# Kernel optimization log

Hardware: AMD Instinct MI355X
Metric: run time of the kernel (lower is better)

## Reference

```python
import jax, jax.numpy as jnp
import numpy as np

B, T_IN, T_OUT, R = 32, 128, 500, 5
MEM_D, ATT, DEC, MEL, SPEC = 256, 256, 256, 128, 513
SPK_N, SPK_D = 5, 32
N_STYLE, STYLE_D, STYLE_ATT = 10, 2, 2
STEPS = T_OUT // R


def _gru(x, h, Wg, bg, Wc, bc):
    # TF GRUCell: r,u gates then candidate with reset-gated state
    gates = jax.nn.sigmoid(jnp.concatenate([x, h], -1) @ Wg + bg)
    r, u = jnp.split(gates, 2, axis=-1)
    c = jnp.tanh(jnp.concatenate([x, r * h], -1) @ Wc + bc)
    return u * h + (1.0 - u) * c


def setup_inputs() -> dict:
    key = jax.random.key(0)
    ks = iter(jax.random.split(key, 48))
    def nrm(shape, s=0.05):
        return (jax.random.normal(next(ks), shape) * s).astype(jnp.float32)
    return dict(
        encoder_output=nrm((B, T_IN, MEM_D), 1.0),
        style_token=nrm((N_STYLE, STYLE_D), 1.0),
        mel_gtruth=nrm((B, T_OUT, MEL), 1.0),
        speaker=jax.random.randint(next(ks), (B,), 0, SPK_N),
        inp_mask=jax.random.randint(next(ks), (B,), T_IN // 2, T_IN + 1),
        spk_embed=nrm((SPK_N, SPK_D)),
        Wp1=nrm((MEL, 256)), bp1=jnp.zeros((256,), jnp.float32),
        Wp2=nrm((256, 128)), bp2=jnp.zeros((128,), jnp.float32),
        Wg_att=nrm((128 + SPK_D + ATT, 2 * ATT)), bg_att=jnp.ones((2 * ATT,), jnp.float32),
        Wc_att=nrm((128 + SPK_D + ATT, ATT)), bc_att=jnp.zeros((ATT,), jnp.float32),
        Wk=nrm((MEM_D, ATT)), Wq=nrm((ATT, ATT)), v_att=nrm((ATT,)),
        Ws_pre=nrm((STYLE_D, STYLE_D)), bs_pre=jnp.zeros((STYLE_D,), jnp.float32),
        Wk_s=nrm((STYLE_D, STYLE_ATT)), Wq_s=nrm((ATT, STYLE_ATT)), v_s=nrm((STYLE_ATT,)),
        Wa=nrm((ATT + SPK_D + MEM_D + STYLE_D, DEC)), ba=jnp.zeros((DEC,), jnp.float32),
        Wg1=nrm((2 * DEC, 2 * DEC)), bg1=jnp.ones((2 * DEC,), jnp.float32),
        Wc1=nrm((2 * DEC, DEC)), bc1=jnp.zeros((DEC,), jnp.float32),
        Wg2=nrm((2 * DEC, 2 * DEC)), bg2=jnp.ones((2 * DEC,), jnp.float32),
        Wc2=nrm((2 * DEC, DEC)), bc2=jnp.zeros((DEC,), jnp.float32),
        Wo=nrm((DEC, MEL * R)), bo=jnp.zeros((MEL * R,), jnp.float32),
        Wspec=nrm((MEL, SPEC)), bspec=jnp.zeros((SPEC,), jnp.float32),
    )


def reference(encoder_output, style_token, mel_gtruth, speaker, inp_mask, spk_embed,
              Wp1, bp1, Wp2, bp2, Wg_att, bg_att, Wc_att, bc_att,
              Wk, Wq, v_att, Ws_pre, bs_pre, Wk_s, Wq_s, v_s,
              Wa, ba, Wg1, bg1, Wc1, bc1, Wg2, bg2, Wc2, bc2,
              Wo, bo, Wspec, bspec):
    mask = jnp.arange(T_IN)[None, :] < inp_mask[:, None]          # [B, T_in]
    keys = encoder_output @ Wk                                     # precomputed attention keys [B,T_in,ATT]
    spk = spk_embed[speaker]                                       # [B, 32]
    mem_style = jax.nn.relu(style_token @ Ws_pre + bs_pre)         # style pre-net [10, 2]
    keys_s = mem_style @ Wk_s                                      # [10, 2]
    # teacher forcing: frame fed at step t is indic[r*t + r - 1] = last gt frame of previous group
    mel_t = jnp.transpose(mel_gtruth, (1, 0, 2))                   # [T_out, B, MEL]
    last = mel_t[R - 1::R]                                         # [STEPS, B, MEL]
    prev = jnp.concatenate([jnp.zeros((1, B, MEL), mel_gtruth.dtype), last[:-1]], 0)

    def step(carry, frame):
        h_att, h1, h2 = carry
        # decoder pre-net (dropout disabled: is_training=False)
        p = jax.nn.relu(frame @ Wp1 + bp1)
        p = jax.nn.relu(p @ Wp2 + bp2)
        h_att = _gru(jnp.concatenate([p, spk], -1), h_att, Wg_att, bg_att, Wc_att, bc_att)
        q = h_att
        # content attention (Bahdanau) over encoder memory
        e = jnp.einsum('bta,a->bt', jnp.tanh(keys + (q @ Wq)[:, None, :]), v_att)
        alpha = jax.nn.softmax(jnp.where(mask, e, -1e9), axis=-1)
        context = jnp.einsum('bt,btd->bd', alpha, encoder_output)
        # style attention over 10 style tokens
        e_s = jnp.einsum('bna,a->bn', jnp.tanh(keys_s[None, :, :] + (q @ Wq_s)[:, None, :]), v_s)
        alpha_s = jax.nn.softmax(e_s, axis=-1)
        context_s = alpha_s @ mem_style                            # [B, 2]
        aco_in = jnp.concatenate([h_att, spk, context, context_s], -1) @ Wa + ba
        # two residual-wrapped GRU layers
        h1n = _gru(aco_in, h1, Wg1, bg1, Wc1, bc1)
        y1 = h1n + aco_in
        h2n = _gru(y1, h2, Wg2, bg2, Wc2, bc2)
        y2 = h2n + y1
        return (h_att, h1n, h2n), (y2 @ Wo + bo, alpha)

    init = (jnp.zeros((B, ATT), jnp.float32),
            jnp.zeros((B, DEC), jnp.float32),
            jnp.zeros((B, DEC), jnp.float32))
    _, (outs, alphas) = jax.lax.scan(step, init, prev)
    output_mel = jnp.transpose(outs, (1, 0, 2)).reshape(B, T_OUT, MEL)
    output_spec = output_mel @ Wspec + bspec
    final_alpha = jnp.transpose(alphas, (1, 0, 2))                 # [B, STEPS, T_in]
    return output_mel, output_spec, final_alpha
```

## Files before the change

kernel.cpp:

```cpp
#include <hip/hip_runtime.h>

typedef unsigned short ushort_t;
typedef unsigned int   uint_t;
typedef unsigned long long u64;
typedef __attribute__((ext_vector_type(8))) short  bf16x8;
typedef __attribute__((ext_vector_type(4))) float  f32x4;

#define B_      32
#define TIN_    128
#define TOUT_   500
#define R_      5
#define STEPS_  100
#define MEL_    128
#define SPEC_   513
#define NWG_    32

#define ZB_SLOTS   0
#define ZB_AH      8192
#define ZB_ARH     24576
#define ZB_AHC     40960
#define ZB_AXH1    73728
#define ZB_AXRH1   106496
#define ZB_AY1H2   139264
#define ZB_AY1RH2  172032
#define ZB_QBUF    204800
#define ZB_UBUF    221184
#define ZB_U1BUF   253952
#define ZB_U2BUF   286720
#define ZB_EBUF    319488
#define ZB_QSBUF   335872
#define ZB_END     435200
#define OFF_SPK2    501760
#define OFF_ACOSPK2 505856
#define OFF_MS2     538624
#define OFF_KS2     539136
#define OFF_PREG2   539648
#define OFF_PREC2   7093248
#define OFF_Y2G     10370048
#define OFF_KEYSP   13646848
#define OFF_ENCP    15744000

__device__ __forceinline__ float bf1(ushort_t u){ return __uint_as_float(((uint_t)u) << 16); }
__device__ __forceinline__ ushort_t f2bf(float f){
    uint_t b = __float_as_uint(f);
    uint_t r = (b + 0x7fffu + ((b >> 16) & 1u)) >> 16;
    return (ushort_t)r;
}
__device__ __forceinline__ float fexp2(float x){ return __builtin_amdgcn_exp2f(x); }
__device__ __forceinline__ float frcp(float x){ return __builtin_amdgcn_rcpf(x); }
__device__ __forceinline__ float sigm_f(float x){ return frcp(1.f + fexp2(-1.44269504f * x)); }
__device__ __forceinline__ float tanh_f(float x){
    float e = fexp2(2.88539008f * x);
    return 1.f - 2.f * frcp(e + 1.f);
}
__device__ __forceinline__ u64 ld8(const void* p){
    return __hip_atomic_load((const u64*)p, __ATOMIC_RELAXED, __HIP_MEMORY_SCOPE_AGENT);
}
__device__ __forceinline__ void st8(void* p, u64 v){
    __hip_atomic_store((u64*)p, v, __ATOMIC_RELAXED, __HIP_MEMORY_SCOPE_AGENT);
}
__device__ __forceinline__ float ld4f(const void* p){
    uint_t u = __hip_atomic_load((const uint_t*)p, __ATOMIC_RELAXED, __HIP_MEMORY_SCOPE_AGENT);
    return __uint_as_float(u);
}
__device__ __forceinline__ void st4f(void* p, float v){
    __hip_atomic_store((uint_t*)p, __float_as_uint(v), __ATOMIC_RELAXED, __HIP_MEMORY_SCOPE_AGENT);
}
__device__ __forceinline__ float u64lo(u64 v){ return __uint_as_float((uint_t)v); }
__device__ __forceinline__ float u64hi(u64 v){ return __uint_as_float((uint_t)(v >> 32)); }
__device__ __forceinline__ u64 pack4(const ushort_t* q){
    return (u64)q[0] | ((u64)q[1] << 16) | ((u64)q[2] << 32) | ((u64)q[3] << 48);
}
__device__ __forceinline__ u64 pack2f(const float* f){
    return (u64)__float_as_uint(f[0]) | ((u64)__float_as_uint(f[1]) << 32);
}
#define CBAR() asm volatile("" ::: "memory")

__global__ __launch_bounds__(256) void k_small(
    const float* __restrict__ st, const float* __restrict__ Ws_pre,
    const float* __restrict__ bs_pre, const float* __restrict__ Wk_s,
    const float* __restrict__ spk_embed, const int* __restrict__ speaker,
    const float* __restrict__ Wa, const float* __restrict__ ba,
    float* __restrict__ spk_sel, float* __restrict__ aco_spk,
    float* __restrict__ ms_g, float* __restrict__ ks_g)
{
    __shared__ float spk_l[B_*32];
    __shared__ float ms_l[20];
    const int tid = threadIdx.x;
    for(int i=tid; i<B_*32; i+=256){
        int b = i >> 5, j = i & 31;
        float v = spk_embed[speaker[b]*32 + j];
        spk_l[i] = v; spk_sel[i] = v;
    }
    if(tid < 20){
        int n = tid >> 1, j = tid & 1;
        float v = st[n*2]*Ws_pre[j] + st[n*2+1]*Ws_pre[2+j] + bs_pre[j];
        v = fmaxf(v, 0.f);
        ms_l[tid] = v; ms_g[tid] = v;
    }
    __syncthreads();
    if(tid < 20){
        int n = tid >> 1, j = tid & 1;
        ks_g[tid] = ms_l[n*2]*Wk_s[j] + ms_l[n*2+1]*Wk_s[2+j];
    }
    for(int i=tid; i<B_*256; i+=256){
        int b = i >> 8, n = i & 255;
        float acc = ba[n];
        #pragma unroll
        for(int k=0;k<32;++k) acc = fmaf(spk_l[b*32+k], Wa[(256+k)*256 + n], acc);
        aco_spk[i] = acc;
    }
}

__global__ __launch_bounds__(256) void k_keys(const float* __restrict__ enc,
                                              const float* __restrict__ Wk,
                                              ushort_t* __restrict__ keysp){
    __shared__ float x16[16][256];
    const int bid = blockIdx.x;
    const int b = bid >> 3, tg = bid & 7, t0 = tg*16;
    const int tid = threadIdx.x;
    for(int i=tid; i<16*256; i+=256){
        int r = i >> 8, k = i & 255;
        x16[r][k] = enc[((size_t)b*TIN_ + t0 + r)*256 + k];
    }
    __syncthreads();
    float acc[16];
    #pragma unroll
    for(int r=0;r<16;++r) acc[r] = 0.f;
    for(int k=0;k<256;++k){
        float w = Wk[k*256 + tid];
        #pragma unroll
        for(int r=0;r<16;++r) acc[r] = fmaf(x16[r][k], w, acc[r]);
    }
    #pragma unroll
    for(int r=0;r<16;++r){
        int t = t0 + r;
        keysp[((size_t)((t>>2)*32 + b)*4 + (t&3))*256 + tid] = f2bf(acc[r]);
    }
}

__global__ __launch_bounds__(256) void k_encperm(const float* __restrict__ enc,
                                                 ushort_t* __restrict__ encp){
    int o = blockIdx.x*256 + threadIdx.x;
    int j = o & 7, t = (o>>3) & 127, b = (o>>10) & 31, wg = o >> 15;
    encp[o] = f2bf(enc[((size_t)b*TIN_ + t)*256 + wg*8 + j]);
}

__global__ __launch_bounds__(256) void k_prenet(
    const float* __restrict__ mg, const float* __restrict__ spk_sel,
    const float* __restrict__ Wp1, const float* __restrict__ bp1,
    const float* __restrict__ Wp2, const float* __restrict__ bp2,
    const float* __restrict__ Wg_att, const float* __restrict__ bg_att,
    const float* __restrict__ Wc_att, const float* __restrict__ bc_att,
    float* __restrict__ preg, float* __restrict__ prec)
{
    __shared__ float fr[16][128];
    __shared__ float p1[16][256];
    __shared__ float p2[16][128];
    __shared__ float spk_l[16][32];
    const int r0 = blockIdx.x * 16;
    const int tid = threadIdx.x;
    for(int i=tid; i<16*128; i+=256){
        int r = i >> 7, mcol = i & 127;
        int row = r0 + r, s = row >> 5, b = row & 31;
        fr[r][mcol] = (s == 0) ? 0.f : mg[((size_t)b*TOUT_ + s*R_ - 1)*MEL_ + mcol];
    }
    for(int i=tid; i<16*32; i+=256){
        int r = i >> 5, j = i & 31;
        spk_l[r][j] = spk_sel[((r0 + r) & 31)*32 + j];
    }
    __syncthreads();
    {
        float acc[16];
        #pragma unroll
        for(int r=0;r<16;++r) acc[r]=0.f;
        for(int k=0;k<128;++k){
            float w = Wp1[k*256 + tid];
            #pragma unroll
            for(int r=0;r<16;++r) acc[r] = fmaf(fr[r][k], w, acc[r]);
        }
        float bb = bp1[tid];
        #pragma unroll
        for(int r=0;r<16;++r) p1[r][tid] = fmaxf(acc[r] + bb, 0.f);
    }
    __syncthreads();
    if(tid < 128){
        float acc[16];
        #pragma unroll
        for(int r=0;r<16;++r) acc[r]=0.f;
        for(int k=0;k<256;++k){
            float w = Wp2[k*128 + tid];
            #pragma unroll
            for(int r=0;r<16;++r) acc[r] = fmaf(p1[r][k], w, acc[r]);
        }
        float bb = bp2[tid];
        #pragma unroll
        for(int r=0;r<16;++r) p2[r][tid] = fmaxf(acc[r] + bb, 0.f);
    }
    __syncthreads();
    {
        float aA[16], aB[16];
        #pragma unroll
        for(int r=0;r<16;++r){ aA[r]=0.f; aB[r]=0.f; }
        for(int k=0;k<128;++k){
            float wA = Wg_att[k*512 + tid], wB = Wg_att[k*512 + tid + 256];
            #pragma unroll
            for(int r=0;r<16;++r){ float pv = p2[r][k]; aA[r]=fmaf(pv,wA,aA[r]); aB[r]=fmaf(pv,wB,aB[r]); }
        }
        for(int k=0;k<32;++k){
            float wA = Wg_att[(128+k)*512 + tid], wB = Wg_att[(128+k)*512 + tid + 256];
            #pragma unroll
            for(int r=0;r<16;++r){ float sv = spk_l[r][k]; aA[r]=fmaf(sv,wA,aA[r]); aB[r]=fmaf(sv,wB,aB[r]); }
        }
        float bA = bg_att[tid], bB = bg_att[tid + 256];
        #pragma unroll
        for(int r=0;r<16;++r){
            preg[(size_t)(r0+r)*512 + tid]       = aA[r] + bA;
            preg[(size_t)(r0+r)*512 + tid + 256] = aB[r] + bB;
        }
    }
    {
        float acc[16];
        #pragma unroll
        for(int r=0;r<16;++r) acc[r]=0.f;
        for(int k=0;k<128;++k){
            float w = Wc_att[k*256 + tid];
            #pragma unroll
            for(int r=0;r<16;++r) acc[r] = fmaf(p2[r][k], w, acc[r]);
        }
        for(int k=0;k<32;++k){
            float w = Wc_att[(128+k)*256 + tid];
            #pragma unroll
            for(int r=0;r<16;++r) acc[r] = fmaf(spk_l[r][k], w, acc[r]);
        }
        float bb = bc_att[tid];
        #pragma unroll
        for(int r=0;r<16;++r) prec[(size_t)(r0+r)*256 + tid] = acc[r] + bb;
    }
}

__device__ __forceinline__ void gridbar(int* slots, int p, int seq, int tid){
    asm volatile("s_waitcnt vmcnt(0)" ::: "memory");
    __syncthreads();
    if(tid == 0)
        __hip_atomic_store(&slots[p*32], seq, __ATOMIC_RELAXED, __HIP_MEMORY_SCOPE_AGENT);
    if(tid < NWG_){
        while(__hip_atomic_load(&slots[tid*32], __ATOMIC_RELAXED, __HIP_MEMORY_SCOPE_AGENT) < seq)
            __builtin_amdgcn_s_sleep(1);
    }
    __syncthreads();
}

__device__ __forceinline__ void loadW(const float* W, int ldw, int rowbase, int nk, int kbase,
                                      int Ktot, int col0, int ncols, ushort_t* lds, int tid){
    for(int e = tid; e < 16*nk; e += 512){
        int col = e & 15, k = e >> 4;
        ushort_t v = 0;
        if(col < ncols) v = f2bf(W[(size_t)(rowbase + k)*ldw + col0 + col]);
        lds[(col*Ktot + kbase + k) ^ ((col & 7) << 3)] = v;
    }
}

template<int K>
__device__ __forceinline__ f32x4 do_gemm(const ushort_t* Ab, const ushort_t* Wl, float* red,
                                         int m, int kq, int lane){
    const int row = m*16 + (lane & 15);
    const int col = lane & 15;
    const int ko  = (lane >> 4) * 8;
    u64 av[K/64];
    #pragma unroll
    for(int t = 0; t < K/128; ++t){
        const int k0 = kq*(K/4) + t*32 + ko;
        av[2*t]   = ld8(Ab + row*K + k0);
        av[2*t+1] = ld8(Ab + row*K + k0 + 4);
    }
    f32x4 acc = {0.f,0.f,0.f,0.f};
    #pragma unroll
    for(int t = 0; t < K/128; ++t){
        const int k0 = kq*(K/4) + t*32 + ko;
        union { u64 q[2]; bf16x8 v; } ua;
        ua.q[0] = av[2*t]; ua.q[1] = av[2*t+1];
        bf16x8 b = *reinterpret_cast<const bf16x8*>(Wl + ((col*K + k0) ^ ((col & 7) << 3)));
        acc = __builtin_amdgcn_mfma_f32_16x16x32_bf16(ua.v, b, acc, 0, 0, 0);
    }
    if(kq > 0) *reinterpret_cast<f32x4*>(red + ((kq-1)*2 + m)*256 + lane*4) = acc;
    __syncthreads();
    if(kq == 0){
        #pragma unroll
        for(int j = 0; j < 3; ++j)
            acc += *reinterpret_cast<const f32x4*>(red + (j*2 + m)*256 + lane*4);
    }
    return acc;
}

__global__ __launch_bounds__(512) void k_scan_coop(
    char* ws,
    const float* __restrict__ Wg_att, const float* __restrict__ Wc_att,
    const float* __restrict__ Wq, const float* __restrict__ Wq_s,
    const float* __restrict__ v_att, const float* __restrict__ v_s,
    const float* __restrict__ Wa,
    const float* __restrict__ Wg1, const float* __restrict__ Wc1,
    const float* __restrict__ Wg2, const float* __restrict__ Wc2,
    const float* __restrict__ bg1, const float* __restrict__ bc1,
    const float* __restrict__ bg2, const float* __restrict__ bc2,
    const int* __restrict__ inp_mask, float* __restrict__ out_alpha)
{
    const int p = blockIdx.x, tid = threadIdx.x;
    const int lane = tid & 63, wv = tid >> 6;
    const int m = wv & 1, kq = wv >> 1;

    int* slots       = (int*)(ws + ZB_SLOTS);
    ushort_t* A_h    = (ushort_t*)(ws + ZB_AH);
    ushort_t* A_rh   = (ushort_t*)(ws + ZB_ARH);
    ushort_t* A_hc   = (ushort_t*)(ws + ZB_AHC);
    ushort_t* A_xh1  = (ushort_t*)(ws + ZB_AXH1);
    ushort_t* A_xrh1 = (ushort_t*)(ws + ZB_AXRH1);
    ushort_t* A_y1h2 = (ushort_t*)(ws + ZB_AY1H2);
    ushort_t* A_y1rh2= (ushort_t*)(ws + ZB_AY1RH2);
    ushort_t* Qbuf   = (ushort_t*)(ws + ZB_QBUF);
    float* ubuf  = (float*)(ws + ZB_UBUF);
    float* u1buf = (float*)(ws + ZB_U1BUF);
    float* u2buf = (float*)(ws + ZB_U2BUF);
    float* ebuf  = (float*)(ws + ZB_EBUF);
    float* qsbuf = (float*)(ws + ZB_QSBUF);
    const float* acospk = (const float*)(ws + OFF_ACOSPK2);
    const float* msg    = (const float*)(ws + OFF_MS2);
    const float* ksg    = (const float*)(ws + OFF_KS2);
    const float* preg   = (const float*)(ws + OFF_PREG2);
    const float* prec   = (const float*)(ws + OFF_PREC2);
    float* y2g          = (float*)(ws + OFF_Y2G);
    const ushort_t* keysp = (const ushort_t*)(ws + OFF_KEYSP);
    const ushort_t* encp  = (const ushort_t*)(ws + OFF_ENCP);

    __shared__ ushort_t wA[16*256], wB[16*256], wC[16*256];
    __shared__ ushort_t wG[16*512], wH[16*512], wI[16*512], wJ[16*512], wK[16*512];
    __shared__ __align__(16) char uni[16384];
    float* red = (float*)uni;
    ushort_t* qlds = (ushort_t*)uni;
    ushort_t* stg  = (ushort_t*)(uni + 8192);
    float*    stgf = (float*)(uni + 10240);
    __shared__ float vatt_l[256];
    __shared__ float msks[48];
    __shared__ float ctxs_l[64];
    __shared__ float acosl[256], acofl[256], y1fl[256];
    __shared__ float hfl[256], h1fl[256], h2fl[256];
    __shared__ float bg1s[16], bc1s[8], bg2s[16], bc2s[8], wasl[16];
    __shared__ float wqs_l[512];
    __shared__ int   maskl[32];

    loadW(Wg_att, 512, 160, 256, 0, 256, p*16, 16, wA, tid);
    loadW(Wc_att, 256, 160, 256, 0, 256, p*8,  8,  wB, tid);
    loadW(Wq,     256, 0,   256, 0, 256, p*8,  8,  wC, tid);
    loadW(Wa,     256, 0,   256, 0,   512, p*8, 8, wG, tid);
    loadW(Wa,     256, 288, 256, 256, 512, p*8, 8, wG, tid);
    loadW(Wg1,    512, 0,   512, 0, 512, p*16, 16, wH, tid);
    loadW(Wc1,    256, 0,   512, 0, 512, p*8,  8,  wI, tid);
    loadW(Wg2,    512, 0,   512, 0, 512, p*16, 16, wJ, tid);
    loadW(Wc2,    256, 0,   512, 0, 512, p*8,  8,  wK, tid);
    if(tid < 256){
        vatt_l[tid] = v_att[tid];
        acosl[tid]  = acospk[(tid>>3)*256 + p*8 + (tid&7)];
        hfl[tid] = 0.f; h1fl[tid] = 0.f; h2fl[tid] = 0.f;
    }
    wqs_l[tid] = Wq_s[tid];
    if(tid < 20) msks[tid] = msg[tid];
    if(tid >= 20 && tid < 40) msks[tid] = ksg[tid-20];
    if(tid == 40) msks[40] = v_s[0];
    if(tid == 41) msks[41] = v_s[1];
    if(tid < 16){ bg1s[tid] = bg1[p*16+tid]; bg2s[tid] = bg2[p*16+tid]; }
    if(tid < 8){ bc1s[tid] = bc1[p*8+tid]; bc2s[tid] = bc2[p*8+tid]; }
    if(tid < 16) wasl[tid] = Wa[(size_t)(544 + (tid & 1))*256 + p*8 + (tid >> 1)];
    if(tid < 32) maskl[tid] = inp_mask[tid];
    __syncthreads();

    int seq = 0;
    for(int s = 0; s < STEPS_; ++s){
        const int sb = s*32;
        const int col = lane & 15;
        const int bbase = m*16 + ((lane>>4)<<2);
        __syncthreads();
        u64 hpre[4];
        if(kq == 0 && p < 16){
            #pragma unroll
            for(int r=0;r<4;++r) hpre[r] = ld8(A_h + (bbase+r)*256 + ((p*16+col) & ~3));
        }
        f32x4 acc = do_gemm<256>(A_h, wA, red, m, kq, lane);
        if(kq == 0){
            const int gcol = p*16 + col;
            if(p < 16){
                #pragma unroll
                for(int r=0;r<4;++r){
                    int b = bbase + r;
                    float g = sigm_f(acc[r] + preg[(size_t)(sb + b)*512 + gcol]);
                    float hb = bf1((ushort_t)(hpre[r] >> ((col & 3)*16)));
                    stg[b*16 + col] = f2bf(g * hb);
                }
                CBAR();
                int c = lane, row2 = m*16 + (c>>2), cg = c & 3;
                st8(A_rh + row2*256 + p*16 + cg*4, pack4(stg + row2*16 + cg*4));
            } else {
                #pragma unroll
                for(int r=0;r<4;++r){
                    int b = bbase + r;
                    stgf[b*16 + col] = sigm_f(acc[r] + preg[(size_t)(sb + b)*512 + gcol]);
                }
                CBAR();
                #pragma unroll
                for(int j=0;j<2;++j){
                    int c = lane*2 + j, row2 = m*16 + (c>>3), cg = c & 7;
                    st8(ubuf + row2*256 + (p-16)*16 + cg*2, pack2f(stgf + row2*16 + cg*2));
                }
            }
        }
        gridbar(slots, p, ++seq, tid);
        float upre[4];
        if(kq == 0 && col < 8){
            #pragma unroll
            for(int r=0;r<4;++r) upre[r] = ld4f(ubuf + (bbase+r)*256 + p*8 + col);
        }
        acc = do_gemm<256>(A_rh, wB, red, m, kq, lane);
        if(kq == 0){
            if(col < 8){
                const int gcol = p*8 + col;
                #pragma unroll
                for(int r=0;r<4;++r){
                    int b = bbase + r;
                    float cc = tanh_f(acc[r] + prec[(size_t)(sb + b)*256 + gcol]);
                    float u  = upre[r];
                    float hn = u*hfl[b*8 + col] + (1.f - u)*cc;
                    hfl[b*8 + col] = hn;
                    stg[b*8 + col] = f2bf(hn);
                }
            }
            CBAR();
            if(lane < 32){
                int c = lane, row2 = m*16 + (c>>1), cg = c & 1;
                u64 v = pack4(stg + row2*8 + cg*4);
                st8(A_h  + row2*256 + p*8 + cg*4, v);
                st8(A_hc + row2*512 + p*8 + cg*4, v);
            }
        }
        gridbar(slots, p, ++seq, tid);
        acc = do_gemm<256>(A_h, wC, red, m, kq, lane);
        if(kq == 0){
            if(col < 8){
                #pragma unroll
                for(int r=0;r<4;++r) stg[(bbase+r)*8 + col] = f2bf(acc[r]);
            }
            CBAR();
            if(lane < 32){
                int c = lane, row2 = m*16 + (c>>1), cg = c & 1;
                st8(Qbuf + row2*256 + p*8 + cg*4, pack4(stg + row2*8 + cg*4));
            }
        }
        if(p == 0){
            int b = tid >> 4, i = tid & 15;
            float q0 = 0.f, q1 = 0.f;
            #pragma unroll
            for(int jc=0;jc<4;++jc){
                u64 h4 = ld8(A_h + b*256 + i*16 + jc*4);
                #pragma unroll
                for(int j=0;j<4;++j){
                    int k = i*16 + jc*4 + j;
                    float hv = bf1((ushort_t)(h4 >> (j*16)));
                    q0 = fmaf(hv, wqs_l[k*2],   q0);
                    q1 = fmaf(hv, wqs_l[k*2+1], q1);
                }
            }
            #pragma unroll
            for(int d=1; d<16; d<<=1){ q0 += __shfl_xor(q0,d,64); q1 += __shfl_xor(q1,d,64); }
            if(i == 0){
                union{ float f[2]; u64 q; } pr; pr.f[0]=q0; pr.f[1]=q1;
                st8(qsbuf + b*2, pr.q);
            }
        }
        gridbar(slots, p, ++seq, tid);
        {
            u64* ql = (u64*)qlds;
            const u64* Qb = (const u64*)Qbuf;
            #pragma unroll
            for(int j=0;j<4;++j) ql[tid + j*512] = ld8(Qb + tid + j*512);
        }
        __syncthreads();
        {
            int b = tid >> 4, tl = (tid >> 2) & 3, q = tid & 3;
            int tg = p*4 + tl;
            const ushort_t* kp = keysp + (((size_t)p*32 + b)*4 + tl)*256 + q*64;
            const ushort_t* qp = qlds + b*256 + q*64;
            float e = 0.f;
            #pragma unroll
            for(int i2=0;i2<8;++i2){
                bf16x8 kv = *(const bf16x8*)(kp + i2*8);
                bf16x8 qv = *(const bf16x8*)(qp + i2*8);
                #pragma unroll
                for(int j=0;j<8;++j){
                    int a = q*64 + i2*8 + j;
                    e = fmaf(vatt_l[a], tanh_f(bf1((ushort_t)kv[j]) + bf1((ushort_t)qv[j])), e);
                }
            }
            e += __shfl_xor(e, 1, 64); e += __shfl_xor(e, 2, 64);
            if(q == 0) st4f(ebuf + b*128 + tg, (tg < maskl[b]) ? e : -1e9f);
        }
        gridbar(slots, p, ++seq, tid);
        {
            int b = tid >> 4, i = tid & 15;
            u64 ea = ld8(ebuf + b*128 + i*8);
            u64 eb = ld8(ebuf + b*128 + i*8 + 2);
            u64 ec = ld8(ebuf + b*128 + i*8 + 4);
            u64 ed = ld8(ebuf + b*128 + i*8 + 6);
            float ev[8] = { u64lo(ea),u64hi(ea),u64lo(eb),u64hi(eb),
                            u64lo(ec),u64hi(ec),u64lo(ed),u64hi(ed) };
            float mx = ev[0];
            #pragma unroll
            for(int j=1;j<8;++j) mx = fmaxf(mx, ev[j]);
            #pragma unroll
            for(int d=1; d<16; d<<=1) mx = fmaxf(mx, __shfl_xor(mx,d,64));
            float a8[8]; float sum = 0.f;
            #pragma unroll
            for(int j=0;j<8;++j){ a8[j] = fexp2((ev[j]-mx)*1.44269504f); sum += a8[j]; }
            #pragma unroll
            for(int d=1; d<16; d<<=1) sum += __shfl_xor(sum,d,64);
            float inv = frcp(sum);
            #pragma unroll
            for(int j=0;j<8;++j) a8[j] *= inv;
            if(p == 1){
                float* oa = out_alpha + ((size_t)b*STEPS_ + s)*TIN_ + i*8;
                #pragma unroll
                for(int j=0;j<8;++j) oa[j] = a8[j];
            }
            float cj[8] = {0,0,0,0,0,0,0,0};
            const ushort_t* ep = encp + (((size_t)p*32 + b)*128 + i*8)*8;
            #pragma unroll
            for(int t2=0;t2<8;++t2){
                bf16x8 ev2 = *(const bf16x8*)(ep + t2*8);
                #pragma unroll
                for(int j=0;j<8;++j) cj[j] = fmaf(a8[t2], bf1((ushort_t)ev2[j]), cj[j]);
            }
            #pragma unroll
            for(int d=1; d<16; d<<=1){
                #pragma unroll
                for(int j=0;j<8;++j) cj[j] += __shfl_xor(cj[j],d,64);
            }
            if(i == 0){
                union{ ushort_t s4[4]; u64 q; } pk0, pk1;
                #pragma unroll
                for(int j=0;j<4;++j){ pk0.s4[j] = f2bf(cj[j]); pk1.s4[j] = f2bf(cj[4+j]); }
                st8(A_hc + b*512 + 256 + p*8,     pk0.q);
                st8(A_hc + b*512 + 256 + p*8 + 4, pk1.q);
            }
        }
        if(tid < 32){
            int b = tid;
            u64 qq = ld8(qsbuf + b*2);
            float q0 = u64lo(qq), q1 = u64hi(qq);
            float es[10]; float mx = -1e30f;
            #pragma unroll
            for(int n=0;n<10;++n){
                float t = msks[40]*tanh_f(msks[20+n*2] + q0) + msks[41]*tanh_f(msks[20+n*2+1] + q1);
                es[n] = t; mx = fmaxf(mx, t);
            }
            float sum = 0.f;
            #pragma unroll
            for(int n=0;n<10;++n){ float pe = fexp2((es[n]-mx)*1.44269504f); es[n]=pe; sum += pe; }
            float inv = frcp(sum); float c0=0.f, c1=0.f;
            #pragma unroll
            for(int n=0;n<10;++n){ float al = es[n]*inv; c0 = fmaf(al, msks[n*2], c0); c1 = fmaf(al, msks[n*2+1], c1); }
            ctxs_l[b*2] = c0; ctxs_l[b*2+1] = c1;
        }
        gridbar(slots, p, ++seq, tid);
        acc = do_gemm<512>(A_hc, wG, red, m, kq, lane);
        if(kq == 0){
            if(col < 8){
                #pragma unroll
                for(int r=0;r<4;++r){
                    int b = bbase + r;
                    float v = acc[r] + acosl[b*8 + col]
                            + ctxs_l[b*2]   * wasl[col*2]
                            + ctxs_l[b*2+1] * wasl[col*2+1];
                    acofl[b*8 + col] = v;
                    stg[b*8 + col] = f2bf(v);
                }
            }
            CBAR();
            if(lane < 32){
                int c = lane, row2 = m*16 + (c>>1), cg = c & 1;
                u64 v = pack4(stg + row2*8 + cg*4);
                st8(A_xh1  + row2*512 + p*8 + cg*4, v);
                st8(A_xrh1 + row2*512 + p*8 + cg*4, v);
            }
        }
        gridbar(slots, p, ++seq, tid);
        if(kq == 0 && p < 16){
            #pragma unroll
            for(int r=0;r<4;++r) hpre[r] = ld8(A_xh1 + (bbase+r)*512 + 256 + ((p*16+col) & ~3));
        }
        acc = do_gemm<512>(A_xh1, wH, red, m, kq, lane);
        if(kq == 0){
            if(p < 16){
                #pragma unroll
                for(int r=0;r<4;++r){
                    int b = bbase + r;
                    float g = sigm_f(acc[r] + bg1s[col]);
                    float hb = bf1((ushort_t)(hpre[r] >> ((col & 3)*16)));
                    stg[b*16 + col] = f2bf(g * hb);
                }
                CBAR();
                int c = lane, row2 = m*16 + (c>>2), cg = c & 3;
                st8(A_xrh1 + row2*512 + 256 + p*16 + cg*4, pack4(stg + row2*16 + cg*4));
            } else {
                #pragma unroll
                for(int r=0;r<4;++r)
                    stgf[(bbase+r)*16 + col] = sigm_f(acc[r] + bg1s[col]);
                CBAR();
                #pragma unroll
                for(int j=0;j<2;++j){
                    int c = lane*2 + j, row2 = m*16 + (c>>3), cg = c & 7;
                    st8(u1buf + row2*256 + (p-16)*16 + cg*2, pack2f(stgf + row2*16 + cg*2));
                }
            }
        }
        gridbar(slots, p, ++seq, tid);
        if(kq == 0 && col < 8){
            #pragma unroll
            for(int r=0;r<4;++r) upre[r] = ld4f(u1buf + (bbase+r)*256 + p*8 + col);
        }
        acc = do_gemm<512>(A_xrh1, wI, red, m, kq, lane);
        if(kq == 0){
            if(col < 8){
                #pragma unroll
                for(int r=0;r<4;++r){
                    int b = bbase + r;
                    float cc = tanh_f(acc[r] + bc1s[col]);
                    float u  = upre[r];
                    float hn = u*h1fl[b*8 + col] + (1.f - u)*cc;
                    h1fl[b*8 + col] = hn;
                    stg[b*8 + col] = f2bf(hn);
                    float y1 = hn + acofl[b*8 + col];
                    y1fl[b*8 + col] = y1;
                    stg[256 + b*8 + col] = f2bf(y1);
                }
            }
            CBAR();
            if(lane < 32){
                int c = lane, row2 = m*16 + (c>>1), cg = c & 1;
                u64 vh = pack4(stg + row2*8 + cg*4);
                u64 vy = pack4(stg + 256 + row2*8 + cg*4);
                st8(A_xh1   + row2*512 + 256 + p*8 + cg*4, vh);
                st8(A_y1h2  + row2*512 + p*8 + cg*4, vy);
                st8(A_y1rh2 + row2*512 + p*8 + cg*4, vy);
            }
        }
        gridbar(slots, p, ++seq, tid);
        if(kq == 0 && p < 16){
            #pragma unroll
            for(int r=0;r<4;++r) hpre[r] = ld8(A_y1h2 + (bbase+r)*512 + 256 + ((p*16+col) & ~3));
        }
        acc = do_gemm<512>(A_y1h2, wJ, red, m, kq, lane);
        if(kq == 0){
            if(p < 16){
                #pragma unroll
                for(int r=0;r<4;++r){
                    int b = bbase + r;
                    float g = sigm_f(acc[r] + bg2s[col]);
                    float hb = bf1((ushort_t)(hpre[r] >> ((col & 3)*16)));
                    stg[b*16 + col] = f2bf(g * hb);
                }
                CBAR();
                int c = lane, row2 = m*16 + (c>>2), cg = c & 3;
                st8(A_y1rh2 + row2*512 + 256 + p*16 + cg*4, pack4(stg + row2*16 + cg*4));
            } else {
                #pragma unroll
                for(int r=0;r<4;++r)
                    stgf[(bbase+r)*16 + col] = sigm_f(acc[r] + bg2s[col]);
                CBAR();
                #pragma unroll
                for(int j=0;j<2;++j){
                    int c = lane*2 + j, row2 = m*16 + (c>>3), cg = c & 7;
                    st8(u2buf + row2*256 + (p-16)*16 + cg*2, pack2f(stgf + row2*16 + cg*2));
                }
            }
        }
        gridbar(slots, p, ++seq, tid);
        if(kq == 0 && col < 8){
            #pragma unroll
            for(int r=0;r<4;++r) upre[r] = ld4f(u2buf + (bbase+r)*256 + p*8 + col);
        }
        acc = do_gemm<512>(A_y1rh2, wK, red, m, kq, lane);
        if(kq == 0){
            if(col < 8){
                const int gcol = p*8 + col;
                #pragma unroll
                for(int r=0;r<4;++r){
                    int b = bbase + r;
                    float cc = tanh_f(acc[r] + bc2s[col]);
                    float u  = upre[r];
                    float hn = u*h2fl[b*8 + col] + (1.f - u)*cc;
                    h2fl[b*8 + col] = hn;
                    stg[b*8 + col] = f2bf(hn);
                    y2g[((size_t)sb + b)*256 + gcol] = hn + y1fl[b*8 + col];
                }
            }
            CBAR();
            if(lane < 32){
                int c = lane, row2 = m*16 + (c>>1), cg = c & 1;
                st8(A_y1h2 + row2*512 + 256 + p*8 + cg*4, pack4(stg + row2*8 + cg*4));
            }
        }
    }
}

__global__ __launch_bounds__(256) void k_omel(const float* __restrict__ y2g,
                                              const float* __restrict__ Wo,
                                              const float* __restrict__ bo,
                                              float* __restrict__ out_mel){
    __shared__ float y8[8][256];
    const int r0 = blockIdx.x * 8;
    const int tid = threadIdx.x;
    for(int i=tid; i<8*256; i+=256){ int r=i>>8, k=i&255; y8[r][k] = y2g[(size_t)(r0+r)*256 + k]; }
    __syncthreads();
    float aA[8], aB[8], aC[8];
    #pragma unroll
    for(int r=0;r<8;++r){ aA[r]=0.f; aB[r]=0.f; aC[r]=0.f; }
    for(int k=0;k<256;++k){
        float wA = Wo[(size_t)k*640 + tid];
        float wB = Wo[(size_t)k*640 + tid + 256];
        float wC = (tid < 128) ? Wo[(size_t)k*640 + tid + 512] : 0.f;
        #pragma unroll
        for(int r=0;r<8;++r){
            float yv = y8[r][k];
            aA[r]=fmaf(yv,wA,aA[r]); aB[r]=fmaf(yv,wB,aB[r]); aC[r]=fmaf(yv,wC,aC[r]);
        }
    }
    float bA = bo[tid], bB = bo[tid+256], bC = (tid<128)? bo[tid+512] : 0.f;
    #pragma unroll
    for(int r=0;r<8;++r){
        int row = r0 + r, s = row >> 5, b = row & 31;
        int mm = tid & 127;
        out_mel[((size_t)b*TOUT_ + s*R_ + (tid>>7))*MEL_ + mm]     = aA[r] + bA;
        out_mel[((size_t)b*TOUT_ + s*R_ + 2 + (tid>>7))*MEL_ + mm] = aB[r] + bB;
        if(tid < 128)
            out_mel[((size_t)b*TOUT_ + s*R_ + 4)*MEL_ + tid]       = aC[r] + bC;
    }
}

__global__ __launch_bounds__(256) void k_spec(const float* __restrict__ out_mel,
                                              const float* __restrict__ Wspec,
                                              const float* __restrict__ bspec,
                                              float* __restrict__ out_spec){
    __shared__ float m8[8][128];
    const int r0 = blockIdx.x * 8;
    const int tid = threadIdx.x;
    for(int i=tid; i<8*128; i+=256){ int r=i>>7, k=i&127; m8[r][k] = out_mel[(size_t)(r0+r)*128 + k]; }
    __syncthreads();
    float aA[8], aB[8], aC[8];
    #pragma unroll
    for(int r=0;r<8;++r){ aA[r]=0.f; aB[r]=0.f; aC[r]=0.f; }
    for(int k=0;k<128;++k){
        float wA = Wspec[(size_t)k*SPEC_ + tid];
        float wB = Wspec[(size_t)k*SPEC_ + 256 + tid];
        float wC = (tid == 0) ? Wspec[(size_t)k*SPEC_ + 512] : 0.f;
        #pragma unroll
        for(int r=0;r<8;++r){
            float mv = m8[r][k];
            aA[r]=fmaf(mv,wA,aA[r]); aB[r]=fmaf(mv,wB,aB[r]); aC[r]=fmaf(mv,wC,aC[r]);
        }
    }
    float bA = bspec[tid], bB = bspec[256+tid];
    #pragma unroll
    for(int r=0;r<8;++r){
        size_t row = (size_t)(r0 + r);
        out_spec[row*SPEC_ + tid]       = aA[r] + bA;
        out_spec[row*SPEC_ + 256 + tid] = aB[r] + bB;
        if(tid == 0) out_spec[row*SPEC_ + 512] = aC[r] + bspec[512];
    }
}

extern "C" void kernel_launch(void* const* d_in, const int* in_sizes, int n_in,
                              void* d_out, int out_size, void* d_ws, size_t ws_size,
                              hipStream_t stream) {
    const float* enc       = (const float*)d_in[0];
    const float* st        = (const float*)d_in[1];
    const float* mg        = (const float*)d_in[2];
    const int*   speaker   = (const int*)  d_in[3];
    const int*   inp_mask  = (const int*)  d_in[4];
    const float* spk_embed = (const float*)d_in[5];
    const float* Wp1=(const float*)d_in[6],  *bp1=(const float*)d_in[7];
    const float* Wp2=(const float*)d_in[8],  *bp2=(const float*)d_in[9];
    const float* Wg_att=(const float*)d_in[10], *bg_att=(const float*)d_in[11];
    const float* Wc_att=(const float*)d_in[12], *bc_att=(const float*)d_in[13];
    const float* Wk=(const float*)d_in[14], *Wq=(const float*)d_in[15], *v_att=(const float*)d_in[16];
    const float* Ws_pre=(const float*)d_in[17], *bs_pre=(const float*)d_in[18];
    const float* Wk_s=(const float*)d_in[19], *Wq_s=(const float*)d_in[20], *v_s=(const float*)d_in[21];
    const float* Wa=(const float*)d_in[22], *ba=(const float*)d_in[23];
    const float* Wg1=(const float*)d_in[24], *bg1=(const float*)d_in[25];
    const float* Wc1=(const float*)d_in[26], *bc1=(const float*)d_in[27];
    const float* Wg2=(const float*)d_in[28], *bg2=(const float*)d_in[29];
    const float* Wc2=(const float*)d_in[30], *bc2=(const float*)d_in[31];
    const float* Wo=(const float*)d_in[32], *bo=(const float*)d_in[33];
    const float* Wspec=(const float*)d_in[34], *bspec=(const float*)d_in[35];

    float* out       = (float*)d_out;
    float* out_mel   = out;
    float* out_spec  = out + 2048000;
    float* out_alpha = out + 10256000;

    char* ws = (char*)d_ws;
    float*    spk_sel = (float*)(ws + OFF_SPK2);
    float*    aco_spk = (float*)(ws + OFF_ACOSPK2);
    float*    ms_g    = (float*)(ws + OFF_MS2);
    float*    ks_g    = (float*)(ws + OFF_KS2);
    float*    preg    = (float*)(ws + OFF_PREG2);
    float*    prec    = (float*)(ws + OFF_PREC2);
    float*    y2g     = (float*)(ws + OFF_Y2G);
    ushort_t* keysp   = (ushort_t*)(ws + OFF_KEYSP);
    ushort_t* encp    = (ushort_t*)(ws + OFF_ENCP);

    hipMemsetAsync(d_ws, 0, ZB_END, stream);

    k_small<<<dim3(1), dim3(256), 0, stream>>>(st, Ws_pre, bs_pre, Wk_s, spk_embed,
                                               speaker, Wa, ba, spk_sel, aco_spk, ms_g, ks_g);
    k_keys   <<<dim3(256),  dim3(256), 0, stream>>>(enc, Wk, keysp);
    k_encperm<<<dim3(4096), dim3(256), 0, stream>>>(enc, encp);
    k_prenet <<<dim3(200),  dim3(256), 0, stream>>>(mg, spk_sel, Wp1, bp1, Wp2, bp2,
                                                    Wg_att, bg_att, Wc_att, bc_att, preg, prec);
    k_scan_coop<<<dim3(NWG_), dim3(512), 0, stream>>>(ws, Wg_att, Wc_att, Wq, Wq_s,
                                                      v_att, v_s, Wa, Wg1, Wc1, Wg2, Wc2,
                                                      bg1, bc1, bg2, bc2, inp_mask, out_alpha);
    k_omel <<<dim3(400),  dim3(256), 0, stream>>>(y2g, Wo, bo, out_mel);
    k_spec <<<dim3(2000), dim3(256), 0, stream>>>(out_mel, Wspec, bspec, out_spec);
}
```

Before: 3.909 ms.

## Compute attention per batch row in each workgroup to drop two grid barriers

The attention stage is repartitioned so that each of the 32 workgroups owns one batch row. Each workgroup computes that row's full query projection (with Wq pre-converted to bf16 in global memory), the energies over all 128 encoder steps, the softmax, the context vector and the style attention. Before, work was split across workgroups by column and time slice, with grid barriers between the query, energy and softmax/context phases. The new layout removes two grid-wide barriers per decoder step, at the cost of redundant per-row work and a scalar GEMV on CUDA cores instead of MFMA. The grid barrier also gains release/acquire ordering, and the keys and encoder buffers switch to plain row-major bf16 layouts.

```diff
diff --git a/kernel.cpp b/kernel.cpp
--- a/kernel.cpp
+++ b/kernel.cpp
@@ -23,22 +23,21 @@
 #define ZB_AXRH1   106496
 #define ZB_AY1H2   139264
 #define ZB_AY1RH2  172032
-#define ZB_QBUF    204800
 #define ZB_UBUF    221184
 #define ZB_U1BUF   253952
 #define ZB_U2BUF   286720
-#define ZB_EBUF    319488
 #define ZB_QSBUF   335872
 #define ZB_END     435200
-#define OFF_SPK2    501760
 #define OFF_ACOSPK2 505856
 #define OFF_MS2     538624
 #define OFF_KS2     539136
+#define OFF_SPK2    501760
 #define OFF_PREG2   539648
 #define OFF_PREC2   7093248
 #define OFF_Y2G     10370048
 #define OFF_KEYSP   13646848
 #define OFF_ENCP    15744000
+#define OFF_WQB     17841152
 
 __device__ __forceinline__ float bf1(ushort_t u){ return __uint_as_float(((uint_t)u) << 16); }
 __device__ __forceinline__ ushort_t f2bf(float f){
@@ -62,9 +61,6 @@
 __device__ __forceinline__ float ld4f(const void* p){
     uint_t u = __hip_atomic_load((const uint_t*)p, __ATOMIC_RELAXED, __HIP_MEMORY_SCOPE_AGENT);
     return __uint_as_float(u);
-}
-__device__ __forceinline__ void st4f(void* p, float v){
-    __hip_atomic_store((uint_t*)p, __float_as_uint(v), __ATOMIC_RELAXED, __HIP_MEMORY_SCOPE_AGENT);
 }
 __device__ __forceinline__ float u64lo(u64 v){ return __uint_as_float((uint_t)v); }
 __device__ __forceinline__ float u64hi(u64 v){ return __uint_as_float((uint_t)(v >> 32)); }
@@ -114,7 +110,7 @@
 
 __global__ __launch_bounds__(256) void k_keys(const float* __restrict__ enc,
                                               const float* __restrict__ Wk,
-                                              ushort_t* __restrict__ keysp){
+                                              ushort_t* __restrict__ keysb){
     __shared__ float x16[16][256];
     const int bid = blockIdx.x;
     const int b = bid >> 3, tg = bid & 7, t0 = tg*16;
@@ -133,17 +129,19 @@
         for(int r=0;r<16;++r) acc[r] = fmaf(x16[r][k], w, acc[r]);
     }
     #pragma unroll
-    for(int r=0;r<16;++r){
-        int t = t0 + r;
-        keysp[((size_t)((t>>2)*32 + b)*4 + (t&3))*256 + tid] = f2bf(acc[r]);
-    }
-}
-
-__global__ __launch_bounds__(256) void k_encperm(const float* __restrict__ enc,
-                                                 ushort_t* __restrict__ encp){
+    for(int r=0;r<16;++r)
+        keysb[((size_t)b*TIN_ + t0 + r)*256 + tid] = f2bf(acc[r]);
+}
+
+__global__ __launch_bounds__(256) void k_cvt_enc(const float* __restrict__ enc,
+                                                 ushort_t* __restrict__ encb){
     int o = blockIdx.x*256 + threadIdx.x;
-    int j = o & 7, t = (o>>3) & 127, b = (o>>10) & 31, wg = o >> 15;
-    encp[o] = f2bf(enc[((size_t)b*TIN_ + t)*256 + wg*8 + j]);
+    encb[o] = f2bf(enc[o]);
+}
+__global__ __launch_bounds__(256) void k_cvt_wq(const float* __restrict__ Wq,
+                                                ushort_t* __restrict__ wqb){
+    int o = blockIdx.x*256 + threadIdx.x;
+    wqb[o] = f2bf(Wq[o]);
 }
 
 __global__ __launch_bounds__(256) void k_prenet(
@@ -243,10 +241,11 @@
     asm volatile("s_waitcnt vmcnt(0)" ::: "memory");
     __syncthreads();
     if(tid == 0)
-        __hip_atomic_store(&slots[p*32], seq, __ATOMIC_RELAXED, __HIP_MEMORY_SCOPE_AGENT);
+        __hip_atomic_store(&slots[p*32], seq, __ATOMIC_RELEASE, __HIP_MEMORY_SCOPE_AGENT);
     if(tid < NWG_){
         while(__hip_atomic_load(&slots[tid*32], __ATOMIC_RELAXED, __HIP_MEMORY_SCOPE_AGENT) < seq)
             __builtin_amdgcn_s_sleep(1);
+        __builtin_amdgcn_fence(__ATOMIC_ACQUIRE, "agent");
     }
     __syncthreads();
 }
@@ -296,7 +295,7 @@
 __global__ __launch_bounds__(512) void k_scan_coop(
     char* ws,
     const float* __restrict__ Wg_att, const float* __restrict__ Wc_att,
-    const float* __restrict__ Wq, const float* __restrict__ Wq_s,
+    const float* __restrict__ Wq_s,
     const float* __restrict__ v_att, const float* __restrict__ v_s,
     const float* __restrict__ Wa,
     const float* __restrict__ Wg1, const float* __restrict__ Wc1,
@@ -317,11 +316,9 @@
     ushort_t* A_xrh1 = (ushort_t*)(ws + ZB_AXRH1);
     ushort_t* A_y1h2 = (ushort_t*)(ws + ZB_AY1H2);
     ushort_t* A_y1rh2= (ushort_t*)(ws + ZB_AY1RH2);
-    ushort_t* Qbuf   = (ushort_t*)(ws + ZB_QBUF);
     float* ubuf  = (float*)(ws + ZB_UBUF);
     float* u1buf = (float*)(ws + ZB_U1BUF);
     float* u2buf = (float*)(ws + ZB_U2BUF);
-    float* ebuf  = (float*)(ws + ZB_EBUF);
     float* qsbuf = (float*)(ws + ZB_QSBUF);
     const float* acospk = (const float*)(ws + OFF_ACOSPK2);
     const float* msg    = (const float*)(ws + OFF_MS2);
@@ -329,14 +326,15 @@
     const float* preg   = (const float*)(ws + OFF_PREG2);
     const float* prec   = (const float*)(ws + OFF_PREC2);
     float* y2g          = (float*)(ws + OFF_Y2G);
-    const ushort_t* keysp = (const ushort_t*)(ws + OFF_KEYSP);
-    const ushort_t* encp  = (const ushort_t*)(ws + OFF_ENCP);
-
-    __shared__ ushort_t wA[16*256], wB[16*256], wC[16*256];
+    const ushort_t* keysb = (const ushort_t*)(ws + OFF_KEYSP);
+    const ushort_t* encb  = (const ushort_t*)(ws + OFF_ENCP);
+    const ushort_t* wqb   = (const ushort_t*)(ws + OFF_WQB);
+
+    __shared__ ushort_t wA[16*256], wB[16*256];
     __shared__ ushort_t wG[16*512], wH[16*512], wI[16*512], wJ[16*512], wK[16*512];
     __shared__ __align__(16) char uni[16384];
     float* red = (float*)uni;
-    ushort_t* qlds = (ushort_t*)uni;
+    float* uf  = (float*)uni;
     ushort_t* stg  = (ushort_t*)(uni + 8192);
     float*    stgf = (float*)(uni + 10240);
     __shared__ float vatt_l[256];
@@ -346,11 +344,9 @@
     __shared__ float hfl[256], h1fl[256], h2fl[256];
     __shared__ float bg1s[16], bc1s[8], bg2s[16], bc2s[8], wasl[16];
     __shared__ float wqs_l[512];
-    __shared__ int   maskl[32];
 
     loadW(Wg_att, 512, 160, 256, 0, 256, p*16, 16, wA, tid);
     loadW(Wc_att, 256, 160, 256, 0, 256, p*8,  8,  wB, tid);
-    loadW(Wq,     256, 0,   256, 0, 256, p*8,  8,  wC, tid);
     loadW(Wa,     256, 0,   256, 0,   512, p*8, 8, wG, tid);
     loadW(Wa,     256, 288, 256, 256, 512, p*8, 8, wG, tid);
     loadW(Wg1,    512, 0,   512, 0, 512, p*16, 16, wH, tid);
@@ -370,7 +366,7 @@
     if(tid < 16){ bg1s[tid] = bg1[p*16+tid]; bg2s[tid] = bg2[p*16+tid]; }
     if(tid < 8){ bc1s[tid] = bc1[p*8+tid]; bc2s[tid] = bc2[p*8+tid]; }
     if(tid < 16) wasl[tid] = Wa[(size_t)(544 + (tid & 1))*256 + p*8 + (tid >> 1)];
-    if(tid < 32) maskl[tid] = inp_mask[tid];
+    const int maskp = inp_mask[p];
     __syncthreads();
 
     int seq = 0;
@@ -441,133 +437,114 @@
             }
         }
         gridbar(slots, p, ++seq, tid);
-        acc = do_gemm<256>(A_h, wC, red, m, kq, lane);
-        if(kq == 0){
-            if(col < 8){
-                #pragma unroll
-                for(int r=0;r<4;++r) stg[(bbase+r)*8 + col] = f2bf(acc[r]);
-            }
+        {
+            float* hrow   = uf;
+            float* qpart  = uf + 256;
+            float* qrow   = uf + 768;
+            float* escore = uf + 1024;
+            float* alphaA = uf + 1152;
+            float* smv    = uf + 1280;
+            float* cpart  = uf + 1536;
+            if(tid < 64){
+                u64 h4 = ld8(A_h + p*256 + tid*4);
+                #pragma unroll
+                for(int j=0;j<4;++j) hrow[tid*4+j] = bf1((ushort_t)(h4 >> (j*16)));
+            }
+            __syncthreads();
+            {
+                int colq = tid & 255, kh = tid >> 8;
+                const ushort_t* wq = wqb + (size_t)(kh*128)*256 + colq;
+                float accq = 0.f;
+                #pragma unroll 4
+                for(int k=0;k<128;++k) accq = fmaf(hrow[kh*128 + k], bf1(wq[(size_t)k*256]), accq);
+                qpart[kh*256 + colq] = accq;
+            }
+            if(tid < 16){
+                float q0s=0.f, q1s=0.f;
+                #pragma unroll
+                for(int kk=0;kk<16;++kk){
+                    int k = tid*16 + kk; float hv = hrow[k];
+                    q0s = fmaf(hv, wqs_l[k*2],   q0s);
+                    q1s = fmaf(hv, wqs_l[k*2+1], q1s);
+                }
+                #pragma unroll
+                for(int d=1; d<16; d<<=1){ q0s += __shfl_xor(q0s,d,64); q1s += __shfl_xor(q1s,d,64); }
+                if(tid == 0){
+                    float es[10]; float mx = -1e30f;
+                    #pragma unroll
+                    for(int n=0;n<10;++n){
+                        float t = msks[40]*tanh_f(msks[20+n*2] + q0s) + msks[41]*tanh_f(msks[20+n*2+1] + q1s);
+                        es[n] = t; mx = fmaxf(mx, t);
+                    }
+                    float sum = 0.f;
+                    #pragma unroll
+                    for(int n=0;n<10;++n){ float pe = fexp2((es[n]-mx)*1.44269504f); es[n]=pe; sum += pe; }
+                    float inv = frcp(sum); float c0=0.f, c1=0.f;
+                    #pragma unroll
+                    for(int n=0;n<10;++n){ float al = es[n]*inv; c0 = fmaf(al, msks[n*2], c0); c1 = fmaf(al, msks[n*2+1], c1); }
+                    float pr2[2] = {c0, c1};
+                    st8(qsbuf + p*2, pack2f(pr2));
+                }
+            }
+            __syncthreads();
+            if(tid < 256) qrow[tid] = qpart[tid] + qpart[256+tid];
+            __syncthreads();
+            {
+                int t = tid >> 2, q = tid & 3;
+                const ushort_t* kp = keysb + ((size_t)(p*TIN_ + t))*256 + q*64;
+                float e = 0.f;
+                #pragma unroll
+                for(int i2=0;i2<8;++i2){
+                    bf16x8 kv = *(const bf16x8*)(kp + i2*8);
+                    #pragma unroll
+                    for(int j=0;j<8;++j){
+                        int a = q*64 + i2*8 + j;
+                        e = fmaf(vatt_l[a], tanh_f(bf1((ushort_t)kv[j]) + qrow[a]), e);
+                    }
+                }
+                e += __shfl_xor(e,1,64); e += __shfl_xor(e,2,64);
+                if(q == 0) escore[t] = (t < maskp) ? e : -1e9f;
+            }
+            __syncthreads();
+            if(tid < 64){
+                float e0 = escore[tid], e1 = escore[tid+64];
+                float mx = fmaxf(e0, e1);
+                #pragma unroll
+                for(int d=1; d<64; d<<=1) mx = fmaxf(mx, __shfl_xor(mx,d,64));
+                float a0 = fexp2((e0-mx)*1.44269504f);
+                float a1 = fexp2((e1-mx)*1.44269504f);
+                alphaA[tid] = a0; alphaA[tid+64] = a1;
+                float ssum = a0 + a1;
+                #pragma unroll
+                for(int d=1; d<64; d<<=1) ssum += __shfl_xor(ssum,d,64);
+                if(tid == 0) smv[0] = frcp(ssum);
+            }
+            __syncthreads();
+            if(tid < 128){
+                float a = alphaA[tid] * smv[0];
+                alphaA[tid] = a;
+                out_alpha[((size_t)p*STEPS_ + s)*TIN_ + tid] = a;
+            }
+            __syncthreads();
+            {
+                int colq = tid & 255, th = tid >> 8;
+                const ushort_t* ep = encb + ((size_t)(p*TIN_ + th*64))*256 + colq;
+                float c = 0.f;
+                #pragma unroll 4
+                for(int tt=0; tt<64; ++tt) c = fmaf(alphaA[th*64+tt], bf1(ep[(size_t)tt*256]), c);
+                cpart[th*256 + colq] = c;
+            }
+            __syncthreads();
+            if(tid < 256) stg[tid] = f2bf(cpart[tid] + cpart[256+tid]);
             CBAR();
-            if(lane < 32){
-                int c = lane, row2 = m*16 + (c>>1), cg = c & 1;
-                st8(Qbuf + row2*256 + p*8 + cg*4, pack4(stg + row2*8 + cg*4));
-            }
-        }
-        if(p == 0){
-            int b = tid >> 4, i = tid & 15;
-            float q0 = 0.f, q1 = 0.f;
-            #pragma unroll
-            for(int jc=0;jc<4;++jc){
-                u64 h4 = ld8(A_h + b*256 + i*16 + jc*4);
-                #pragma unroll
-                for(int j=0;j<4;++j){
-                    int k = i*16 + jc*4 + j;
-                    float hv = bf1((ushort_t)(h4 >> (j*16)));
-                    q0 = fmaf(hv, wqs_l[k*2],   q0);
-                    q1 = fmaf(hv, wqs_l[k*2+1], q1);
-                }
-            }
-            #pragma unroll
-            for(int d=1; d<16; d<<=1){ q0 += __shfl_xor(q0,d,64); q1 += __shfl_xor(q1,d,64); }
-            if(i == 0){
-                union{ float f[2]; u64 q; } pr; pr.f[0]=q0; pr.f[1]=q1;
-                st8(qsbuf + b*2, pr.q);
-            }
+            __syncthreads();
+            if(tid < 64) st8(A_hc + p*512 + 256 + tid*4, pack4(stg + tid*4));
         }
         gridbar(slots, p, ++seq, tid);
-        {
-            u64* ql = (u64*)qlds;
-            const u64* Qb = (const u64*)Qbuf;
-            #pragma unroll
-            for(int j=0;j<4;++j) ql[tid + j*512] = ld8(Qb + tid + j*512);
-        }
-        __syncthreads();
-        {
-            int b = tid >> 4, tl = (tid >> 2) & 3, q = tid & 3;
-            int tg = p*4 + tl;
-            const ushort_t* kp = keysp + (((size_t)p*32 + b)*4 + tl)*256 + q*64;
-            const ushort_t* qp = qlds + b*256 + q*64;
-            float e = 0.f;
-            #pragma unroll
-            for(int i2=0;i2<8;++i2){
-                bf16x8 kv = *(const bf16x8*)(kp + i2*8);
-                bf16x8 qv = *(const bf16x8*)(qp + i2*8);
-                #pragma unroll
-                for(int j=0;j<8;++j){
-                    int a = q*64 + i2*8 + j;
-                    e = fmaf(vatt_l[a], tanh_f(bf1((ushort_t)kv[j]) + bf1((ushort_t)qv[j])), e);
-                }
-            }
-            e += __shfl_xor(e, 1, 64); e += __shfl_xor(e, 2, 64);
-            if(q == 0) st4f(ebuf + b*128 + tg, (tg < maskl[b]) ? e : -1e9f);
-        }
-        gridbar(slots, p, ++seq, tid);
-        {
-            int b = tid >> 4, i = tid & 15;
-            u64 ea = ld8(ebuf + b*128 + i*8);
-            u64 eb = ld8(ebuf + b*128 + i*8 + 2);
-            u64 ec = ld8(ebuf + b*128 + i*8 + 4);
-            u64 ed = ld8(ebuf + b*128 + i*8 + 6);
-            float ev[8] = { u64lo(ea),u64hi(ea),u64lo(eb),u64hi(eb),
-                            u64lo(ec),u64hi(ec),u64lo(ed),u64hi(ed) };
-            float mx = ev[0];
-            #pragma unroll
-            for(int j=1;j<8;++j) mx = fmaxf(mx, ev[j]);
-            #pragma unroll
-            for(int d=1; d<16; d<<=1) mx = fmaxf(mx, __shfl_xor(mx,d,64));
-            float a8[8]; float sum = 0.f;
-            #pragma unroll
-            for(int j=0;j<8;++j){ a8[j] = fexp2((ev[j]-mx)*1.44269504f); sum += a8[j]; }
-            #pragma unroll
-            for(int d=1; d<16; d<<=1) sum += __shfl_xor(sum,d,64);
-            float inv = frcp(sum);
-            #pragma unroll
-            for(int j=0;j<8;++j) a8[j] *= inv;
-            if(p == 1){
-                float* oa = out_alpha + ((size_t)b*STEPS_ + s)*TIN_ + i*8;
-                #pragma unroll
-                for(int j=0;j<8;++j) oa[j] = a8[j];
-            }
-            float cj[8] = {0,0,0,0,0,0,0,0};
-            const ushort_t* ep = encp + (((size_t)p*32 + b)*128 + i*8)*8;
-            #pragma unroll
-            for(int t2=0;t2<8;++t2){
-                bf16x8 ev2 = *(const bf16x8*)(ep + t2*8);
-                #pragma unroll
-                for(int j=0;j<8;++j) cj[j] = fmaf(a8[t2], bf1((ushort_t)ev2[j]), cj[j]);
-            }
-            #pragma unroll
-            for(int d=1; d<16; d<<=1){
-                #pragma unroll
-                for(int j=0;j<8;++j) cj[j] += __shfl_xor(cj[j],d,64);
-            }
-            if(i == 0){
-                union{ ushort_t s4[4]; u64 q; } pk0, pk1;
-                #pragma unroll
-                for(int j=0;j<4;++j){ pk0.s4[j] = f2bf(cj[j]); pk1.s4[j] = f2bf(cj[4+j]); }
-                st8(A_hc + b*512 + 256 + p*8,     pk0.q);
-                st8(A_hc + b*512 + 256 + p*8 + 4, pk1.q);
-            }
-        }
         if(tid < 32){
-            int b = tid;
-            u64 qq = ld8(qsbuf + b*2);
-            float q0 = u64lo(qq), q1 = u64hi(qq);
-            float es[10]; float mx = -1e30f;
-            #pragma unroll
-            for(int n=0;n<10;++n){
-                float t = msks[40]*tanh_f(msks[20+n*2] + q0) + msks[41]*tanh_f(msks[20+n*2+1] + q1);
-                es[n] = t; mx = fmaxf(mx, t);
-            }
-            float sum = 0.f;
-            #pragma unroll
-            for(int n=0;n<10;++n){ float pe = fexp2((es[n]-mx)*1.44269504f); es[n]=pe; sum += pe; }
-            float inv = frcp(sum); float c0=0.f, c1=0.f;
-            #pragma unroll
-            for(int n=0;n<10;++n){ float al = es[n]*inv; c0 = fmaf(al, msks[n*2], c0); c1 = fmaf(al, msks[n*2+1], c1); }
-            ctxs_l[b*2] = c0; ctxs_l[b*2+1] = c1;
-        }
-        gridbar(slots, p, ++seq, tid);
+            u64 qq = ld8(qsbuf + tid*2);
+            ctxs_l[tid*2] = u64lo(qq); ctxs_l[tid*2+1] = u64hi(qq);
+        }
         acc = do_gemm<512>(A_hc, wG, red, m, kq, lane);
         if(kq == 0){
             if(col < 8){
@@ -812,18 +789,20 @@
     float*    preg    = (float*)(ws + OFF_PREG2);
     float*    prec    = (float*)(ws + OFF_PREC2);
     float*    y2g     = (float*)(ws + OFF_Y2G);
-    ushort_t* keysp   = (ushort_t*)(ws + OFF_KEYSP);
-    ushort_t* encp    = (ushort_t*)(ws + OFF_ENCP);
+    ushort_t* keysb   = (ushort_t*)(ws + OFF_KEYSP);
+    ushort_t* encb    = (ushort_t*)(ws + OFF_ENCP);
+    ushort_t* wqb     = (ushort_t*)(ws + OFF_WQB);
 
     hipMemsetAsync(d_ws, 0, ZB_END, stream);
 
     k_small<<<dim3(1), dim3(256), 0, stream>>>(st, Ws_pre, bs_pre, Wk_s, spk_embed,
                                                speaker, Wa, ba, spk_sel, aco_spk, ms_g, ks_g);
-    k_keys   <<<dim3(256),  dim3(256), 0, stream>>>(enc, Wk, keysp);
-    k_encperm<<<dim3(4096), dim3(256), 0, stream>>>(enc, encp);
+    k_keys   <<<dim3(256),  dim3(256), 0, stream>>>(enc, Wk, keysb);
+    k_cvt_enc<<<dim3(4096), dim3(256), 0, stream>>>(enc, encb);
+    k_cvt_wq <<<dim3(256),  dim3(256), 0, stream>>>(Wq, wqb);
     k_prenet <<<dim3(200),  dim3(256), 0, stream>>>(mg, spk_sel, Wp1, bp1, Wp2, bp2,
                                                     Wg_att, bg_att, Wc_att, bc_att, preg, prec);
-    k_scan_coop<<<dim3(NWG_), dim3(512), 0, stream>>>(ws, Wg_att, Wc_att, Wq, Wq_s,
+    k_scan_coop<<<dim3(NWG_), dim3(512), 0, stream>>>(ws, Wg_att, Wc_att, Wq_s,
                                                       v_att, v_s, Wa, Wg1, Wc1, Wg2, Wc2,
                                                       bg1, bc1, bg2, bc2, inp_mask, out_alpha);
     k_omel <<<dim3(400),  dim3(256), 0, stream>>>(y2g, Wo, bo, out_mel);
```

Measured after the change: 4.136 ms. +5.8%, slower.
